# Kernel optimization log

Hardware: AMD Instinct MI355X
Metric: run time of the kernel (lower is better)

The kernel has to match this reference:

```python
import jax, jax.numpy as jnp
import numpy as np
from jax import lax

# dims: T timesteps, CIN=6 DoG channels, HxW image; F conv filters, K kernel
T, CIN, H, W_IN = 15, 6, 512, 512
F, K, PAD = 64, 5, 2
THRESH = 15.0
K_WTA, RADIUS = 5, 2  # self.k1, self.r1


def setup_inputs() -> dict:
    key = jax.random.key(0)
    k1, k2 = jax.random.split(key)
    # cumulative binary spike wave: once a unit spikes it stays 1 (SpykeTorch convention)
    ev = (jax.random.uniform(k1, (T, CIN, H, W_IN)) < 0.02).astype(jnp.float32)
    x = jnp.clip(jnp.cumsum(ev, axis=0), 0.0, 1.0)
    w = 0.8 + 0.05 * jax.random.normal(k2, (F, CIN, K, K), dtype=jnp.float32)
    return {"x": x, "w": w}


def _pool_pad(x, pad):
    # sf.pooling(x, 2, 2): max-pool 2x2 stride 2; sf.pad: zero pad
    x = lax.reduce_window(x, -jnp.inf, lax.max, (1, 1, 2, 2), (1, 1, 2, 2), 'VALID')
    return jnp.pad(x, ((0, 0), (0, 0), (pad, pad), (pad, pad)))


def _fire(pot, thr):
    # sf.fire(pot, thr, True): zero sub-threshold potentials, spikes = sign
    tp = jnp.where(pot < thr, 0.0, pot)
    return jnp.sign(tp), tp


def _pointwise_inhibition(pot):
    # keep, per spatial site, only the feature with the earliest (then strongest) spike
    T_ = pot.shape[0]
    max_vals = jnp.max(pot, axis=1, keepdims=True)      # [T,1,H,W]
    max_idx = jnp.argmax(pot, axis=1, keepdims=True)    # [T,1,H,W]
    clamp = jnp.sign(max_vals)                          # 1 where any feature active
    earliest = jnp.clip(T_ - jnp.sum(clamp, axis=0, keepdims=True), 0, T_ - 1).astype(jnp.int32)  # [1,1,H,W]
    winners = jnp.take_along_axis(max_idx, earliest, axis=0)  # [1,1,H,W] winning feature
    has_spike = clamp[-1:]                              # [1,1,H,W] any spike by last step
    ch = jnp.arange(pot.shape[1]).reshape(1, -1, 1, 1)
    coef = jnp.where(ch == winners, has_spike, 0.0)     # scatter of winner coeff
    return pot * coef


def _get_k_winners(pot, spikes, k, radius):
    # NMS-like radius-based k-winners-take-all over [F,H,W]
    T_ = pot.shape[0]
    earliest = jnp.clip(T_ - jnp.sum(spikes, axis=0, keepdims=True), 0, T_ - 1).astype(jnp.int32)
    values = jnp.take_along_axis(pot, earliest, axis=0)  # potential at earliest spike
    trunc = spikes * values
    v = jnp.max(trunc) * T_  # large bias favoring earlier spikes
    total = jnp.sum(trunc + spikes * v, axis=0)          # [F,H,W]
    Fc, Hh, Ww = total.shape
    feat = jnp.arange(Fc).reshape(-1, 1, 1)
    row = jnp.arange(Hh).reshape(1, -1, 1)
    col = jnp.arange(Ww).reshape(1, 1, -1)
    winners = []
    for _ in range(k):  # small fixed k (5), fine to unroll
        idx = jnp.argmax(total)
        val = jnp.reshape(total, (-1,))[idx]
        f, r, c = jnp.unravel_index(idx, total.shape)
        active = val != 0
        win = jnp.where(active, jnp.stack([f, r, c]).astype(jnp.int32),
                        jnp.full((3,), -1, jnp.int32))
        winners.append(win)
        suppress = (feat == f) | ((jnp.abs(row - r) <= radius) & (jnp.abs(col - c) <= radius))
        total = jnp.where(active & suppress, 0.0, total)
    return jnp.stack(winners)  # [k,3] with -1 rows when fewer winners exist


def reference(x, w):
    inp = _pool_pad(x, PAD)  # [T,6,260,260]
    pot = lax.conv_general_dilated(inp, w, (1, 1), 'VALID',
                                   dimension_numbers=('NCHW', 'OIHW', 'NCHW'))  # [T,F,256,256]
    spk, pot = _fire(pot, THRESH)
    pot = _pointwise_inhibition(pot)
    spk = jnp.sign(pot)
    winners = _get_k_winners(pot, spk, K_WTA, RADIUS)
    return spk, winners
```

## Files before the change

kernel.cpp:

```cpp
#include <hip/hip_runtime.h>
#include <hip/hip_bf16.h>

#define T_ 15
#define CIN_ 6
#define F_ 64
#define HW_ 256
#define PW_ 260
#define THRESH_ 15.0f
#define TAU_NEVER 15

typedef float v4f __attribute__((ext_vector_type(4)));


__global__ __launch_bounds__(256) void pool_tau(const float* __restrict__ x,
                                                unsigned char* __restrict__ tau,
                                                unsigned int* __restrict__ gmaxp) {
    int idx = blockIdx.x * 256 + threadIdx.x;
    if (idx == 0) *gmaxp = 0u;
    if (idx >= CIN_ * PW_ * PW_) return;
    int xx = idx % PW_;
    int rest = idx / PW_;
    int yy = rest % PW_;
    int c = rest / PW_;
    unsigned char tv = TAU_NEVER;
    if (xx >= 2 && xx < 258 && yy >= 2 && yy < 258) {
        int i = yy - 2, j = xx - 2;
        const float* b0 = x + ((size_t)c * 512 + 2 * i) * 512 + 2 * j;
        const size_t tstride = (size_t)CIN_ * 512 * 512;
        const float* b = b0 + 14 * tstride;
        float2 a = *(const float2*)b;
        float2 d = *(const float2*)(b + 512);
        if (a.x > 0.f || a.y > 0.f || d.x > 0.f || d.y > 0.f) {
            int lo = 0, hi = 14;
            while (lo < hi) {
                int mid = (lo + hi) >> 1;
                const float* bm = b0 + (size_t)mid * tstride;
                float2 am = *(const float2*)bm;
                float2 dm = *(const float2*)(bm + 512);
                bool on = (am.x > 0.f || am.y > 0.f || dm.x > 0.f || dm.y > 0.f);
                if (on) hi = mid; else lo = mid + 1;
            }
            tv = (unsigned char)lo;
        }
    }
    tau[idx] = tv;
}

__global__ __launch_bounds__(256, 3) void phaseA(const unsigned char* __restrict__ tau,
                                                 const float* __restrict__ w,
                                                 int* __restrict__ rec_wch,
                                                 float* __restrict__ rec_val,
                                                 int* __restrict__ rec_e,
                                                 unsigned int* __restrict__ gmaxp) {
    __shared__ float wl2[150 * 64];
    __shared__ unsigned char tw[CIN_ * 144];
    __shared__ float wmax[4];

    const int tid = threadIdx.x;
    const int lane = tid & 63;
    const int g = tid >> 6;
    const int gx = (g & 1) * 4;
    const int gy = (g >> 1) * 4;
    const int px0 = blockIdx.x * 8;
    const int py0 = blockIdx.y * 8;

    for (int idx = tid; idx < 9600; idx += 256) {
        int k = idx >> 6, f = idx & 63;
        wl2[idx] = w[f * 150 + k];
    }
    for (int idx = tid; idx < CIN_ * 144; idx += 256) {
        int c = idx / 144;
        int rem = idx - c * 144;
        int r = rem / 12;
        int xx = rem - r * 12;
        tw[idx] = tau[(c * PW_ + (py0 + r)) * PW_ + (px0 + xx)];
    }
    __syncthreads();

    unsigned int done = 0;
    int myw = -1, mye = T_;
    float myv = 0.0f;
    float wavemax = 0.0f;

    for (int t = 0; t < T_; ++t) {
        float acc[16];
#pragma unroll
        for (int i = 0; i < 16; ++i) acc[i] = 0.0f;

        for (int c = 0; c < CIN_; ++c) {
            float win[8][8];
            const unsigned char* tb = &tw[c * 144 + gy * 12 + gx];
#pragma unroll
            for (int r = 0; r < 8; ++r) {
                unsigned int lo = *(const unsigned int*)(tb + r * 12);
                unsigned int hi = *(const unsigned int*)(tb + r * 12 + 4);
#pragma unroll
                for (int b = 0; b < 4; ++b) {
                    win[r][b]     = (((lo >> (8 * b)) & 0xFF) <= (unsigned)t) ? 1.0f : 0.0f;
                    win[r][4 + b] = (((hi >> (8 * b)) & 0xFF) <= (unsigned)t) ? 1.0f : 0.0f;
                }
            }
#pragma unroll
            for (int ki = 0; ki < 5; ++ki)
#pragma unroll
                for (int kj = 0; kj < 5; ++kj) {
                    float wv = wl2[((c * 25 + ki * 5 + kj) << 6) + lane];
#pragma unroll
                    for (int py = 0; py < 4; ++py)
#pragma unroll
                        for (int px = 0; px < 4; ++px)
                            acc[py * 4 + px] += win[py + ki][px + kj] * wv;
                }
        }

#pragma unroll
        for (int i = 0; i < 16; ++i) {
            if (done & (1u << i)) continue;
            float v = acc[i];
            v = (v < THRESH_) ? 0.0f : v;
            if (__any(v > 0.0f)) {
                unsigned long long key =
                    ((unsigned long long)__float_as_uint(v) << 6) | (unsigned)(63 - lane);
#pragma unroll
                for (int m = 1; m < 64; m <<= 1) {
                    unsigned long long o = __shfl_xor(key, m, 64);
                    if (o > key) key = o;
                }
                float mv = __uint_as_float((unsigned int)(key >> 6));
                int wf = 63 - (int)(key & 63ULL);
                done |= (1u << i);
                if (lane == i) { myw = wf; myv = mv; mye = t; }
                wavemax = fmaxf(wavemax, mv);
            }
        }
        if (done == 0xFFFFu) break;
    }

    if (lane < 16) {
        int py = lane >> 2, px = lane & 3;
        int p = (py0 + gy + py) * HW_ + (px0 + gx + px);
        rec_wch[p] = myw;
        rec_val[p] = myv;
        rec_e[p] = mye;
    }
    if (lane == 0) wmax[g] = wavemax;
    __syncthreads();
    if (tid == 0) {
        float m = fmaxf(fmaxf(wmax[0], wmax[1]), fmaxf(wmax[2], wmax[3]));
        if (m > 0.0f) atomicMax(gmaxp, __float_as_uint(m));
    }
}

__global__ __launch_bounds__(256) void render_keys(const int* __restrict__ rec_wch,
                                                   const float* __restrict__ rec_val,
                                                   const int* __restrict__ rec_e,
                                                   const unsigned int* __restrict__ gmaxp,
                                                   unsigned long long* __restrict__ keys,
                                                   float* __restrict__ out) {
    const int tid = threadIdx.x;
    const int t = blockIdx.y;
    const int px = blockIdx.x * 1024 + tid * 4;

    int4 wch4 = *(const int4*)(rec_wch + px);
    int4 e4   = *(const int4*)(rec_e + px);
    int s0 = (wch4.x >= 0 && t >= e4.x) ? wch4.x : -1;
    int s1 = (wch4.y >= 0 && t >= e4.y) ? wch4.y : -1;
    int s2 = (wch4.z >= 0 && t >= e4.z) ? wch4.z : -1;
    int s3 = (wch4.w >= 0 && t >= e4.w) ? wch4.w : -1;

    float* base = out + (((size_t)t * F_) << 16) + px;
#pragma unroll
    for (int f = 0; f < F_; ++f) {
        v4f v;
        v.x = (f == s0) ? 1.0f : 0.0f;
        v.y = (f == s1) ? 1.0f : 0.0f;
        v.z = (f == s2) ? 1.0f : 0.0f;
        v.w = (f == s3) ? 1.0f : 0.0f;
        __builtin_nontemporal_store(v, (v4f*)(base + ((size_t)f << 16)));
    }

    if (t == 0) {
        float g = __uint_as_float(*gmaxp);
        float v15 = 15.0f * g;
        float4 val4 = *(const float4*)(rec_val + px);
#pragma unroll
        for (int q = 0; q < 4; ++q) {
            int wch = (q == 0) ? wch4.x : (q == 1) ? wch4.y : (q == 2) ? wch4.z : wch4.w;
            float val = (q == 0) ? val4.x : (q == 1) ? val4.y : (q == 2) ? val4.z : val4.w;
            int e = (q == 0) ? e4.x : (q == 1) ? e4.y : (q == 2) ? e4.z : e4.w;
            unsigned long long key = 0ULL;
            if (wch >= 0) {
                float bse = val + v15;
                float tot = 0.0f;
                for (int tt = e; tt < T_; ++tt) tot += bse;
                if (tot > 0.0f) {
                    int fl = (wch << 16) | (px + q);
                    key = ((unsigned long long)__float_as_uint(tot) << 32)
                        | (0x7fffffffu - (unsigned int)fl);
                }
            }
            keys[px + q] = key;
        }
    }
}

__global__ __launch_bounds__(1024) void select5(const unsigned long long* __restrict__ keys,
                                                float* __restrict__ out) {
    __shared__ unsigned long long wred[16];
    __shared__ int swf[5], swr[5], swc[5];
    const int tid = threadIdx.x;
    const int lane = tid & 63;
    const int wid = tid >> 6;

    unsigned long long t0 = 0, t1 = 0, t2 = 0, t3 = 0;
    int nz = 0;
#pragma unroll
    for (int k8 = 0; k8 < 8; ++k8) {
        unsigned long long b0 = keys[(k8 * 8 + 0) * 1024 + tid];
        unsigned long long b1 = keys[(k8 * 8 + 1) * 1024 + tid];
        unsigned long long b2 = keys[(k8 * 8 + 2) * 1024 + tid];
        unsigned long long b3 = keys[(k8 * 8 + 3) * 1024 + tid];
        unsigned long long b4 = keys[(k8 * 8 + 4) * 1024 + tid];
        unsigned long long b5 = keys[(k8 * 8 + 5) * 1024 + tid];
        unsigned long long b6 = keys[(k8 * 8 + 6) * 1024 + tid];
        unsigned long long b7 = keys[(k8 * 8 + 7) * 1024 + tid];
#pragma unroll
        for (int j = 0; j < 8; ++j) {
            unsigned long long kk =
                (j == 0) ? b0 : (j == 1) ? b1 : (j == 2) ? b2 : (j == 3) ? b3 :
                (j == 4) ? b4 : (j == 5) ? b5 : (j == 6) ? b6 : b7;
            nz += (kk != 0ULL);
            if (kk > t3) {
                if (kk > t0)      { t3 = t2; t2 = t1; t1 = t0; t0 = kk; }
                else if (kk > t1) { t3 = t2; t2 = t1; t1 = kk; }
                else if (kk > t2) { t3 = t2; t2 = kk; }
                else              { t3 = kk; }
            }
        }
    }

    for (int round = 0; round < 5; ++round) {
        int pf0 = -9, pr0 = -9000, pc0 = -9000;
        int pf1 = -9, pr1 = -9000, pc1 = -9000;
        int pf2 = -9, pr2 = -9000, pc2 = -9000;
        int pf3 = -9, pr3 = -9000, pc3 = -9000;
        if (round > 0) { pf0 = swf[0]; pr0 = swr[0]; pc0 = swc[0]; }
        if (round > 1) { pf1 = swf[1]; pr1 = swr[1]; pc1 = swc[1]; }
        if (round > 2) { pf2 = swf[2]; pr2 = swr[2]; pc2 = swc[2]; }
        if (round > 3) { pf3 = swf[3]; pr3 = swr[3]; pc3 = swc[3]; }

        unsigned long long best = 0ULL;
        int nsup = 0;
#pragma unroll
        for (int j = 0; j < 4; ++j) {
            unsigned long long kk = (j == 0) ? t0 : (j == 1) ? t1 : (j == 2) ? t2 : t3;
            if (kk == 0ULL) continue;
            int fl = 0x7fffffff - (int)(unsigned int)(kk & 0xffffffffu);
            int f = fl >> 16, r = (fl >> 8) & 255, c = fl & 255;
            bool sup = (f == pf0) || (abs(r - pr0) <= 2 && abs(c - pc0) <= 2);
            sup = sup || (f == pf1) || (abs(r - pr1) <= 2 && abs(c - pc1) <= 2);
            sup = sup || (f == pf2) || (abs(r - pr2) <= 2 && abs(c - pc2) <= 2);
            sup = sup || (f == pf3) || (abs(r - pr3) <= 2 && abs(c - pc3) <= 2);
            if (sup) ++nsup;
            else if (kk > best) best = kk;
        }
        if (best == 0ULL && nsup == 4 && nz > 4) {
            for (int k = 0; k < 64; ++k) {
                unsigned long long kk = keys[k * 1024 + tid];
                if (kk == 0ULL) continue;
                int fl = 0x7fffffff - (int)(unsigned int)(kk & 0xffffffffu);
                int f = fl >> 16, r = (fl >> 8) & 255, c = fl & 255;
                bool sup = (f == pf0) || (abs(r - pr0) <= 2 && abs(c - pc0) <= 2);
                sup = sup || (f == pf1) || (abs(r - pr1) <= 2 && abs(c - pc1) <= 2);
                sup = sup || (f == pf2) || (abs(r - pr2) <= 2 && abs(c - pc2) <= 2);
                sup = sup || (f == pf3) || (abs(r - pr3) <= 2 && abs(c - pc3) <= 2);
                if (!sup && kk > best) best = kk;
            }
        }

#pragma unroll
        for (int m = 1; m < 64; m <<= 1) {
            unsigned long long o = __shfl_xor(best, m, 64);
            if (o > best) best = o;
        }
        if (lane == 0) wred[wid] = best;
        __syncthreads();
        if (tid == 0) {
            unsigned long long b = wred[0];
#pragma unroll
            for (int j = 1; j < 16; ++j)
                if (wred[j] > b) b = wred[j];
            float* wout = out + (size_t)T_ * F_ * HW_ * HW_ + round * 3;
            if (b != 0ULL) {
                int fl = 0x7fffffff - (int)(unsigned int)(b & 0xffffffffu);
                int f = fl >> 16, r = (fl >> 8) & 255, c = fl & 255;
                swf[round] = f; swr[round] = r; swc[round] = c;
                wout[0] = (float)f; wout[1] = (float)r; wout[2] = (float)c;
            } else {
                swf[round] = -9; swr[round] = -9000; swc[round] = -9000;
                wout[0] = -1.0f; wout[1] = -1.0f; wout[2] = -1.0f;
            }
        }
        __syncthreads();
    }
}

extern "C" void kernel_launch(void* const* d_in, const int* in_sizes, int n_in,
                              void* d_out, int out_size, void* d_ws, size_t ws_size,
                              hipStream_t stream) {
    const float* x = (const float*)d_in[0];
    const float* w = (const float*)d_in[1];
    float* out = (float*)d_out;

    char* wsc = (char*)d_ws;
    unsigned char* tau = (unsigned char*)wsc;
    size_t off = (size_t)CIN_ * PW_ * PW_;
    int* rec_wch = (int*)(wsc + off);        off += 65536 * sizeof(int);
    float* rec_val = (float*)(wsc + off);    off += 65536 * sizeof(float);
    int* rec_e = (int*)(wsc + off);          off += 65536 * sizeof(int);
    unsigned long long* keys = (unsigned long long*)(wsc + off);  off += 65536 * sizeof(unsigned long long);
    unsigned int* gmaxp = (unsigned int*)(wsc + off);

    pool_tau<<<(CIN_ * PW_ * PW_ + 255) / 256, 256, 0, stream>>>(x, tau, gmaxp);
    phaseA<<<dim3(32, 32), 256, 0, stream>>>(tau, w, rec_wch, rec_val, rec_e, gmaxp);
    render_keys<<<dim3(64, 15), 256, 0, stream>>>(rec_wch, rec_val, rec_e, gmaxp, keys, out);
    select5<<<1, 1024, 0, stream>>>(keys, out);
}
```

Before: 479.2 us.

## Fuse pooling/first-spike-time computation into conv kernel and use SWAR threshold test

```diff
diff --git a/kernel.cpp b/kernel.cpp
--- a/kernel.cpp
+++ b/kernel.cpp
@@ -12,41 +12,7 @@
 typedef float v4f __attribute__((ext_vector_type(4)));
 
 
-__global__ __launch_bounds__(256) void pool_tau(const float* __restrict__ x,
-                                                unsigned char* __restrict__ tau,
-                                                unsigned int* __restrict__ gmaxp) {
-    int idx = blockIdx.x * 256 + threadIdx.x;
-    if (idx == 0) *gmaxp = 0u;
-    if (idx >= CIN_ * PW_ * PW_) return;
-    int xx = idx % PW_;
-    int rest = idx / PW_;
-    int yy = rest % PW_;
-    int c = rest / PW_;
-    unsigned char tv = TAU_NEVER;
-    if (xx >= 2 && xx < 258 && yy >= 2 && yy < 258) {
-        int i = yy - 2, j = xx - 2;
-        const float* b0 = x + ((size_t)c * 512 + 2 * i) * 512 + 2 * j;
-        const size_t tstride = (size_t)CIN_ * 512 * 512;
-        const float* b = b0 + 14 * tstride;
-        float2 a = *(const float2*)b;
-        float2 d = *(const float2*)(b + 512);
-        if (a.x > 0.f || a.y > 0.f || d.x > 0.f || d.y > 0.f) {
-            int lo = 0, hi = 14;
-            while (lo < hi) {
-                int mid = (lo + hi) >> 1;
-                const float* bm = b0 + (size_t)mid * tstride;
-                float2 am = *(const float2*)bm;
-                float2 dm = *(const float2*)(bm + 512);
-                bool on = (am.x > 0.f || am.y > 0.f || dm.x > 0.f || dm.y > 0.f);
-                if (on) hi = mid; else lo = mid + 1;
-            }
-            tv = (unsigned char)lo;
-        }
-    }
-    tau[idx] = tv;
-}
-
-__global__ __launch_bounds__(256, 3) void phaseA(const unsigned char* __restrict__ tau,
+__global__ __launch_bounds__(256, 3) void phaseA(const float* __restrict__ x,
                                                  const float* __restrict__ w,
                                                  int* __restrict__ rec_wch,
                                                  float* __restrict__ rec_val,
@@ -68,12 +34,35 @@
         int k = idx >> 6, f = idx & 63;
         wl2[idx] = w[f * 150 + k];
     }
+
     for (int idx = tid; idx < CIN_ * 144; idx += 256) {
         int c = idx / 144;
         int rem = idx - c * 144;
         int r = rem / 12;
         int xx = rem - r * 12;
-        tw[idx] = tau[(c * PW_ + (py0 + r)) * PW_ + (px0 + xx)];
+        int gpy = py0 + r - 2;
+        int gpx = px0 + xx - 2;
+        unsigned char tv = TAU_NEVER;
+        if (gpy >= 0 && gpy < HW_ && gpx >= 0 && gpx < HW_) {
+            const float* b0 = x + ((size_t)c * 512 + 2 * gpy) * 512 + 2 * gpx;
+            const size_t tstride = (size_t)CIN_ * 512 * 512;
+            const float* b = b0 + 14 * tstride;
+            float2 a = *(const float2*)b;
+            float2 d = *(const float2*)(b + 512);
+            if (a.x > 0.f || a.y > 0.f || d.x > 0.f || d.y > 0.f) {
+                int lo = 0, hi = 14;
+                while (lo < hi) {
+                    int mid = (lo + hi) >> 1;
+                    const float* bm = b0 + (size_t)mid * tstride;
+                    float2 am = *(const float2*)bm;
+                    float2 dm = *(const float2*)(bm + 512);
+                    bool on = (am.x > 0.f || am.y > 0.f || dm.x > 0.f || dm.y > 0.f);
+                    if (on) hi = mid; else lo = mid + 1;
+                }
+                tv = (unsigned char)lo;
+            }
+        }
+        tw[idx] = tv;
     }
     __syncthreads();
 
@@ -87,6 +76,8 @@
 #pragma unroll
         for (int i = 0; i < 16; ++i) acc[i] = 0.0f;
 
+        const unsigned int K = (127u - (unsigned)t) * 0x01010101u;
+
         for (int c = 0; c < CIN_; ++c) {
             float win[8][8];
             const unsigned char* tb = &tw[c * 144 + gy * 12 + gx];
@@ -94,10 +85,12 @@
             for (int r = 0; r < 8; ++r) {
                 unsigned int lo = *(const unsigned int*)(tb + r * 12);
                 unsigned int hi = *(const unsigned int*)(tb + r * 12 + 4);
+                unsigned int onlo = (~(lo + K) >> 7) & 0x01010101u;
+                unsigned int onhi = (~(hi + K) >> 7) & 0x01010101u;
 #pragma unroll
                 for (int b = 0; b < 4; ++b) {
-                    win[r][b]     = (((lo >> (8 * b)) & 0xFF) <= (unsigned)t) ? 1.0f : 0.0f;
-                    win[r][4 + b] = (((hi >> (8 * b)) & 0xFF) <= (unsigned)t) ? 1.0f : 0.0f;
+                    win[r][b]     = (float)((onlo >> (8 * b)) & 0xFFu);
+                    win[r][4 + b] = (float)((onhi >> (8 * b)) & 0xFFu);
                 }
             }
 #pragma unroll
@@ -313,16 +306,15 @@
     float* out = (float*)d_out;
 
     char* wsc = (char*)d_ws;
-    unsigned char* tau = (unsigned char*)wsc;
-    size_t off = (size_t)CIN_ * PW_ * PW_;
+    size_t off = 0;
     int* rec_wch = (int*)(wsc + off);        off += 65536 * sizeof(int);
     float* rec_val = (float*)(wsc + off);    off += 65536 * sizeof(float);
     int* rec_e = (int*)(wsc + off);          off += 65536 * sizeof(int);
     unsigned long long* keys = (unsigned long long*)(wsc + off);  off += 65536 * sizeof(unsigned long long);
     unsigned int* gmaxp = (unsigned int*)(wsc + off);
 
-    pool_tau<<<(CIN_ * PW_ * PW_ + 255) / 256, 256, 0, stream>>>(x, tau, gmaxp);
-    phaseA<<<dim3(32, 32), 256, 0, stream>>>(tau, w, rec_wch, rec_val, rec_e, gmaxp);
+    hipMemsetAsync(gmaxp, 0, sizeof(unsigned int), stream);
+    phaseA<<<dim3(32, 32), 256, 0, stream>>>(x, w, rec_wch, rec_val, rec_e, gmaxp);
     render_keys<<<dim3(64, 15), 256, 0, stream>>>(rec_wch, rec_val, rec_e, gmaxp, keys, out);
     select5<<<1, 1024, 0, stream>>>(keys, out);
 }
```

Result: no change. 474.8 us (-0.9%).
